# Performance work log

Measured on AMD Instinct MI355X. Metric: run time of the kernel, lower is better.

## Reference

```python
import jax, jax.numpy as jnp
import numpy as np

# Paged/ragged causal prefill attention (FlashInfer wrapper.run semantics),
# modeled as equal-length batched causal GQA attention.
B, S = 2, 2048          # batch, seq_len (T = B*S tokens, flattened)
H, HKV, D = 32, 8, 128  # query heads, kv heads, head dim
G = H // HKV            # GQA group size
SCALE = 0.08838834764831845  # 1/sqrt(D)


def setup_inputs() -> dict:
    key = jax.random.key(0)
    kq, kk, kv = jax.random.split(key, 3)
    q = jax.random.normal(kq, (B * S, H * D), dtype=jnp.float32)
    k = jax.random.normal(kk, (B * S, HKV * D), dtype=jnp.float32)
    v = jax.random.normal(kv, (B * S, HKV * D), dtype=jnp.float32)
    return {"q": q, "k": k, "v": v}


def reference(q, k, v):
    # q: [T, H*D] -> [B, S, HKV, G, D]; k, v: [T, HKV*D] -> [B, S, HKV, D]
    qh = q.reshape(B, S, HKV, G, D)
    kh = k.reshape(B, S, HKV, D)
    vh = v.reshape(B, S, HKV, D)
    # GQA attention scores: [B, HKV, G, Sq, Sk]
    scores = jnp.einsum('bqhgd,bkhd->bhgqk', qh, kh) * SCALE
    causal = jnp.tril(jnp.ones((S, S), dtype=bool))  # query attends to keys <= its position
    scores = jnp.where(causal, scores, jnp.finfo(scores.dtype).min)
    probs = jax.nn.softmax(scores, axis=-1)
    out = jnp.einsum('bhgqk,bkhd->bqhgd', probs, vh)
    # back to flattened token layout [T, H*D]
    return out.reshape(B * S, H * D)
```

## Files before the change

kernel.cpp:

```cpp
#include <hip/hip_runtime.h>


#define B_   2
#define S_   2048
#define H_   32
#define HKV_ 8
#define D_   128
#define SCALEF 0.08838834764831845f
#define COEF  (SCALEF * 1.44269504088896340736f)
#define DEFER_THR 8.0f

typedef float          f32x4 __attribute__((ext_vector_type(4)));
typedef __bf16         bf16x4 __attribute__((ext_vector_type(4)));
typedef __bf16         bf16x8 __attribute__((ext_vector_type(8)));
typedef unsigned short u16x8 __attribute__((ext_vector_type(8)));

#define MFMA16(a, b, c) __builtin_amdgcn_mfma_f32_16x16x32_bf16((a), (b), (c), 0, 0, 0)

#if defined(__has_builtin)
#if __has_builtin(__builtin_amdgcn_exp2f)
#define EXP2F(x) __builtin_amdgcn_exp2f(x)
#endif
#endif
#ifndef EXP2F
#define EXP2F(x) exp2f(x)
#endif

static __device__ __forceinline__ unsigned short f2bf(float f) {
  unsigned int u = __builtin_bit_cast(unsigned int, f);
  u = (u + 0x7fffu + ((u >> 16) & 1u)) >> 16;
  return (unsigned short)u;
}

static __device__ __forceinline__ void load_lds16(const void* g, void* l) {
  __builtin_amdgcn_global_load_lds(
      (const __attribute__((address_space(1))) void*)g,
      (__attribute__((address_space(3))) void*)l, 16, 0, 0);
}

static __device__ __forceinline__ float swz_x16(float v) {
  return __builtin_bit_cast(
      float, __builtin_amdgcn_ds_swizzle(__builtin_bit_cast(int, v), 0x401F));
}
static __device__ __forceinline__ float bperm_f(int byteaddr, float v) {
  return __builtin_bit_cast(
      float,
      __builtin_amdgcn_ds_bpermute(byteaddr, __builtin_bit_cast(int, v)));
}

__global__ __launch_bounds__(256) void k_convert_kernel(
    const float* __restrict__ k, unsigned short* __restrict__ kbf) {
  int t = blockIdx.x * 256 + threadIdx.x;
  int o = t * 8;
  int d = o & (D_ - 1);
  int s = (o >> 7) & (S_ - 1);
  int bh = o >> 18;
  int b = bh >> 3, hkv = bh & 7;
  const float* src = k + (size_t)(b * S_ + s) * (HKV_ * D_) + hkv * D_ + d;
  f32x4 x0 = *(const f32x4*)src;
  f32x4 x1 = *(const f32x4*)(src + 4);
  u16x8 w;
  w[0] = f2bf(x0[0]); w[1] = f2bf(x0[1]); w[2] = f2bf(x0[2]); w[3] = f2bf(x0[3]);
  w[4] = f2bf(x1[0]); w[5] = f2bf(x1[1]); w[6] = f2bf(x1[2]); w[7] = f2bf(x1[3]);
  *(u16x8*)(kbf + o) = w;
}

__global__ __launch_bounds__(256) void vt_transpose_kernel(
    const float* __restrict__ v, unsigned short* __restrict__ vt) {
  __shared__ float tile[32][65];
  const int tid = threadIdx.x;
  const int s0 = blockIdx.x * 64;
  const int d0 = blockIdx.y * 32;
  const int bh = blockIdx.z;
  const float* src = v + (size_t)(bh >> 3) * S_ * (HKV_ * D_) + (bh & 7) * D_;
#pragma unroll
  for (int it = 0; it < 8; ++it) {
    int idx = it * 256 + tid;
    int sl = idx >> 5, dl = idx & 31;
    tile[dl][sl] = src[(size_t)(s0 + sl) * (HKV_ * D_) + d0 + dl];
  }
  __syncthreads();
  unsigned int* dst = (unsigned int*)vt;
#pragma unroll
  for (int it = 0; it < 4; ++it) {
    int idx = it * 256 + tid;
    int dl = idx >> 5, sp = idx & 31;
    unsigned int w = (unsigned int)f2bf(tile[dl][2 * sp]) |
                     ((unsigned int)f2bf(tile[dl][2 * sp + 1]) << 16);
    dst[(((size_t)bh * D_ + d0 + dl) * S_ + s0 + 2 * sp) >> 1] = w;
  }
}

#define PSTR 36

__global__ __launch_bounds__(256, 4) void attn_kernel(
    const float* __restrict__ qg, const unsigned short* __restrict__ kbfg,
    const unsigned short* __restrict__ vtg, float* __restrict__ outg) {
  __shared__ unsigned short KL[2][32 * 128];
  __shared__ unsigned short VL[2][128 * 32];
  __shared__ unsigned short PL[4][16 * PSTR];

  const int tid = threadIdx.x;
  const int wave = tid >> 6, lane = tid & 63;
  const int l15 = lane & 15, quad = lane >> 4;
  const int a32 = ((lane ^ 32) << 2);
  const int rowa = quad << 4;

  const int xb = (int)blockIdx.x;
  const int b = (int)(blockIdx.y >> 5), h = (int)(blockIdx.y & 31);
  const int hkv = h >> 2;

  const unsigned short* kbf = kbfg + (size_t)(b * HKV_ + hkv) * S_ * D_;
  const unsigned short* vtb = vtg + (size_t)(b * HKV_ + hkv) * D_ * S_;

  const f32x4 zero4 = {0.f, 0.f, 0.f, 0.f};
  const float NEG_INF = -__builtin_huge_valf();

  auto stage = [&](int kt, int buf) {
#pragma unroll
    for (int j = 0; j < 2; ++j) {
      int si = wave * 128 + j * 64 + lane;
      int kr = si >> 4, pc = si & 15;
      int lc = pc ^ (kr & 15);
      load_lds16(kbf + (size_t)(kt * 32 + kr) * D_ + lc * 8,
                 &KL[buf][(wave * 128 + j * 64) * 8]);
    }
#pragma unroll
    for (int j = 0; j < 2; ++j) {
      int si = wave * 128 + j * 64 + lane;
      int dr = si >> 2, pc = si & 3;
      int lc = pc ^ ((dr >> 1) & 3);
      load_lds16(vtb + (size_t)dr * S_ + kt * 32 + lc * 8,
                 &VL[buf][(wave * 128 + j * 64) * 8]);
    }
  };

  for (int ph = 0; ph < 2; ++ph) {
    const int qb = ph ? (31 - xb) : xb;
    const int qbase = qb * 64 + wave * 16;
    const int qgp = qbase + l15;

    bf16x8 qf[4];
#pragma unroll
    for (int ch = 0; ch < 4; ++ch) {
      const float* p = qg + (size_t)(b * S_ + qbase + l15) * (H_ * D_) +
                       h * D_ + ch * 32 + quad * 8;
      f32x4 x0 = *(const f32x4*)p;
      f32x4 x1 = *(const f32x4*)(p + 4);
      bf16x8 t;
      t[0] = (__bf16)(x0[0] * COEF); t[1] = (__bf16)(x0[1] * COEF);
      t[2] = (__bf16)(x0[2] * COEF); t[3] = (__bf16)(x0[3] * COEF);
      t[4] = (__bf16)(x1[0] * COEF); t[5] = (__bf16)(x1[1] * COEF);
      t[6] = (__bf16)(x1[2] * COEF); t[7] = (__bf16)(x1[3] * COEF);
      qf[ch] = t;
    }

    f32x4 acc[8];
#pragma unroll
    for (int dt = 0; dt < 8; ++dt) acc[dt] = zero4;
    float mrow = NEG_INF;
    float lsum = 0.f;

    const int nkt = qb * 2 + 2;

    stage(0, 0);
    __syncthreads();

#define KITER(KT, CUR)                                                        \
  do {                                                                        \
    const int kt_ = (KT);                                                     \
    if (kt_ + 1 < nkt) stage(kt_ + 1, (CUR) ^ 1);                             \
    if (kt_ * 32 <= qbase + 15) {                                             \
      f32x4 sc[2] = {zero4, zero4};                                           \
      __builtin_amdgcn_s_setprio(1);                                          \
      _Pragma("unroll") for (int h2 = 0; h2 < 2; ++h2) {                      \
        const int row = h2 * 16 + l15;                                        \
        _Pragma("unroll") for (int ch = 0; ch < 4; ++ch) {                    \
          const int pc = (ch * 4 + quad) ^ l15;               \
          u16x8 kf = *(const u16x8*)&KL[(CUR)][row * D_ + pc * 8];            \
          sc[h2] = MFMA16(__builtin_bit_cast(bf16x8, kf), qf[ch], sc[h2]);    \
        }                                                                     \
      }                                                                       \
      __builtin_amdgcn_s_setprio(0);                                          \
      const int kb0 = kt_ * 32;                                               \
          \
      _Pragma("unroll") for (int h2 = 0; h2 < 2; ++h2) {                      \
        if (kb0 + h2 * 16 + 15 > qbase) {                                     \
          int kb2 = kb0 + h2 * 16 + quad * 4;                                 \
          _Pragma("unroll") for (int r = 0; r < 4; ++r) {                     \
            if (kb2 + r > qgp) sc[h2][r] = NEG_INF;                           \
          }                                                                   \
        }                                                                     \
      }                                                                       \
         \
      float l8 = fmaxf(fmaxf(fmaxf(sc[0][0], sc[0][1]),                       \
                             fmaxf(sc[0][2], sc[0][3])),                      \
                       fmaxf(fmaxf(sc[1][0], sc[1][1]),                       \
                             fmaxf(sc[1][2], sc[1][3])));                     \
      if (!__all(l8 <= mrow + DEFER_THR)) {                                   \
        float t = fmaxf(l8, swz_x16(l8));             \
        t = fmaxf(t, bperm_f(a32, t));                                        \
        float mn = fmaxf(mrow, t);                                            \
        float al = EXP2F(mrow - mn);                                          \
        mrow = mn;                                                            \
        lsum *= al;                                                           \
        f32x4 av;       \
        _Pragma("unroll") for (int r = 0; r < 4; ++r)                         \
            av[r] = bperm_f(rowa + (r << 2), al);                             \
        _Pragma("unroll") for (int dt = 0; dt < 8; ++dt)                      \
            _Pragma("unroll") for (int r = 0; r < 4; ++r)                     \
                acc[dt][r] *= av[r];                                          \
      }                                                                       \
                         \
      _Pragma("unroll") for (int h2 = 0; h2 < 2; ++h2)                        \
          _Pragma("unroll") for (int r = 0; r < 4; ++r)                       \
              sc[h2][r] = EXP2F(sc[h2][r] - mrow);                            \
      lsum += ((sc[0][0] + sc[0][1]) + (sc[0][2] + sc[0][3])) +               \
              ((sc[1][0] + sc[1][1]) + (sc[1][2] + sc[1][3]));                \
            \
      {                                                                       \
        bf16x4 w0, w1;                                                        \
        w0[0] = (__bf16)sc[0][0]; w0[1] = (__bf16)sc[0][1];                   \
        w0[2] = (__bf16)sc[0][2]; w0[3] = (__bf16)sc[0][3];                   \
        w1[0] = (__bf16)sc[1][0]; w1[1] = (__bf16)sc[1][1];                   \
        w1[2] = (__bf16)sc[1][2]; w1[3] = (__bf16)sc[1][3];                   \
        *(bf16x4*)&PL[wave][l15 * PSTR + quad * 4] = w0;                      \
        *(bf16x4*)&PL[wave][l15 * PSTR + 16 + quad * 4] = w1;                 \
      }                                                                       \
             \
      {                                                                       \
        bf16x4 p0 = *(const bf16x4*)&PL[wave][l15 * PSTR + quad * 8];         \
        bf16x4 p1 = *(const bf16x4*)&PL[wave][l15 * PSTR + quad * 8 + 4];     \
        bf16x8 pb = __builtin_shufflevector(p0, p1, 0, 1, 2, 3, 4, 5, 6, 7);  \
        const int vsw = (quad ^ ((l15 >> 1) & 3)) * 8;                        \
        __builtin_amdgcn_s_setprio(1);                                        \
        _Pragma("unroll") for (int dt = 0; dt < 8; ++dt) {                    \
          u16x8 vf = *(const u16x8*)&VL[(CUR)][(dt * 16 + l15) * 32 + vsw];   \
          acc[dt] = MFMA16(pb, __builtin_bit_cast(bf16x8, vf), acc[dt]);      \
        }                                                                     \
        __builtin_amdgcn_s_setprio(0);                                        \
      }                                                                       \
    }                                                                         \
    __syncthreads();  \
  } while (0)

    for (int kt = 0; kt < nkt; kt += 2) {
      KITER(kt, 0);
      KITER(kt + 1, 1);
    }
#undef KITER

    float s = lsum;
    s += swz_x16(s);
    s += bperm_f(a32, s);
    float linv = 1.0f / s;
    f32x4 inv;
#pragma unroll
    for (int r = 0; r < 4; ++r) inv[r] = bperm_f(rowa + (r << 2), linv);
#pragma unroll
    for (int dt = 0; dt < 8; ++dt)
#pragma unroll
      for (int r = 0; r < 4; ++r)
        outg[(size_t)(b * S_ + qbase + quad * 4 + r) * (H_ * D_) +
             h * D_ + dt * 16 + l15] = acc[dt][r] * inv[r];
  }
}

extern "C" void kernel_launch(void* const* d_in, const int* in_sizes, int n_in,
                              void* d_out, int out_size, void* d_ws,
                              size_t ws_size, hipStream_t stream) {
  const float* q = (const float*)d_in[0];
  const float* k = (const float*)d_in[1];
  const float* v = (const float*)d_in[2];
  float* out = (float*)d_out;
  unsigned short* kws = (unsigned short*)d_ws;
  unsigned short* vtws = kws + (size_t)B_ * HKV_ * S_ * D_;

  k_convert_kernel<<<(B_ * S_ * HKV_ * D_ / 8) / 256, 256, 0, stream>>>(k, kws);

  dim3 g1(S_ / 64, D_ / 32, B_ * HKV_);
  vt_transpose_kernel<<<g1, 256, 0, stream>>>(v, vtws);

  dim3 g2(16, B_ * H_);
  attn_kernel<<<g2, 256, 0, stream>>>(q, kws, vtws, out);
}
```

Before: 233.2 us.

## Permute K rows to keep P in registers, fuse prep kernels, remap blocks to XCDs

New measurement: 244.5 us. +4.9%, slower.

```diff
diff --git a/kernel.cpp b/kernel.cpp
--- a/kernel.cpp
+++ b/kernel.cpp
@@ -48,57 +48,56 @@
       __builtin_amdgcn_ds_bpermute(byteaddr, __builtin_bit_cast(int, v)));
 }
 
-__global__ __launch_bounds__(256) void k_convert_kernel(
-    const float* __restrict__ k, unsigned short* __restrict__ kbf) {
-  int t = blockIdx.x * 256 + threadIdx.x;
-  int o = t * 8;
-  int d = o & (D_ - 1);
-  int s = (o >> 7) & (S_ - 1);
-  int bh = o >> 18;
-  int b = bh >> 3, hkv = bh & 7;
-  const float* src = k + (size_t)(b * S_ + s) * (HKV_ * D_) + hkv * D_ + d;
-  f32x4 x0 = *(const f32x4*)src;
-  f32x4 x1 = *(const f32x4*)(src + 4);
-  u16x8 w;
-  w[0] = f2bf(x0[0]); w[1] = f2bf(x0[1]); w[2] = f2bf(x0[2]); w[3] = f2bf(x0[3]);
-  w[4] = f2bf(x1[0]); w[5] = f2bf(x1[1]); w[6] = f2bf(x1[2]); w[7] = f2bf(x1[3]);
-  *(u16x8*)(kbf + o) = w;
-}
-
-__global__ __launch_bounds__(256) void vt_transpose_kernel(
-    const float* __restrict__ v, unsigned short* __restrict__ vt) {
+__global__ __launch_bounds__(256) void prep_kernel(
+    const float* __restrict__ k, const float* __restrict__ v,
+    unsigned short* __restrict__ kbf, unsigned short* __restrict__ vt) {
   __shared__ float tile[32][65];
   const int tid = threadIdx.x;
-  const int s0 = blockIdx.x * 64;
-  const int d0 = blockIdx.y * 32;
-  const int bh = blockIdx.z;
-  const float* src = v + (size_t)(bh >> 3) * S_ * (HKV_ * D_) + (bh & 7) * D_;
-#pragma unroll
-  for (int it = 0; it < 8; ++it) {
-    int idx = it * 256 + tid;
-    int sl = idx >> 5, dl = idx & 31;
-    tile[dl][sl] = src[(size_t)(s0 + sl) * (HKV_ * D_) + d0 + dl];
+  const int gid = (int)blockIdx.x;
+  if (gid < 2048) {
+    int t = gid * 256 + tid;
+    int o = t * 8;
+    int d = o & (D_ - 1);
+    int s = (o >> 7) & (S_ - 1);
+    int bh = o >> 18;
+    int b = bh >> 3, hkv = bh & 7;
+    const float* src = k + (size_t)(b * S_ + s) * (HKV_ * D_) + hkv * D_ + d;
+    f32x4 x0 = *(const f32x4*)src;
+    f32x4 x1 = *(const f32x4*)(src + 4);
+    u16x8 w;
+    w[0] = f2bf(x0[0]); w[1] = f2bf(x0[1]); w[2] = f2bf(x0[2]); w[3] = f2bf(x0[3]);
+    w[4] = f2bf(x1[0]); w[5] = f2bf(x1[1]); w[6] = f2bf(x1[2]); w[7] = f2bf(x1[3]);
+    *(u16x8*)(kbf + o) = w;
+  } else {
+    const int t = gid - 2048;
+    const int s0 = (t & 31) * 64;
+    const int d0 = ((t >> 5) & 3) * 32;
+    const int bh = t >> 7;
+    const float* src = v + (size_t)(bh >> 3) * S_ * (HKV_ * D_) + (bh & 7) * D_;
+#pragma unroll
+    for (int it = 0; it < 8; ++it) {
+      int idx = it * 256 + tid;
+      int sl = idx >> 5, dl = idx & 31;
+      tile[dl][sl] = src[(size_t)(s0 + sl) * (HKV_ * D_) + d0 + dl];
+    }
+    __syncthreads();
+    unsigned int* dst = (unsigned int*)vt;
+#pragma unroll
+    for (int it = 0; it < 4; ++it) {
+      int idx = it * 256 + tid;
+      int dl = idx >> 5, sp = idx & 31;
+      unsigned int w = (unsigned int)f2bf(tile[dl][2 * sp]) |
+                       ((unsigned int)f2bf(tile[dl][2 * sp + 1]) << 16);
+      dst[(((size_t)bh * D_ + d0 + dl) * S_ + s0 + 2 * sp) >> 1] = w;
+    }
   }
-  __syncthreads();
-  unsigned int* dst = (unsigned int*)vt;
-#pragma unroll
-  for (int it = 0; it < 4; ++it) {
-    int idx = it * 256 + tid;
-    int dl = idx >> 5, sp = idx & 31;
-    unsigned int w = (unsigned int)f2bf(tile[dl][2 * sp]) |
-                     ((unsigned int)f2bf(tile[dl][2 * sp + 1]) << 16);
-    dst[(((size_t)bh * D_ + d0 + dl) * S_ + s0 + 2 * sp) >> 1] = w;
-  }
-}
-
-#define PSTR 36
-
-__global__ __launch_bounds__(256, 4) void attn_kernel(
+}
+
+__global__ __launch_bounds__(256, 5) void attn_kernel(
     const float* __restrict__ qg, const unsigned short* __restrict__ kbfg,
     const unsigned short* __restrict__ vtg, float* __restrict__ outg) {
   __shared__ unsigned short KL[2][32 * 128];
   __shared__ unsigned short VL[2][128 * 32];
-  __shared__ unsigned short PL[4][16 * PSTR];
 
   const int tid = threadIdx.x;
   const int wave = tid >> 6, lane = tid & 63;
@@ -106,9 +105,14 @@
   const int a32 = ((lane ^ 32) << 2);
   const int rowa = quad << 4;
 
-  const int xb = (int)blockIdx.x;
-  const int b = (int)(blockIdx.y >> 5), h = (int)(blockIdx.y & 31);
-  const int hkv = h >> 2;
+  const int id = (int)blockIdx.x + 16 * (int)blockIdx.y;
+  const int xcd = id & 7, slot = id >> 3;
+  const int bhkv = xcd * 2 + (slot >> 6);
+  const int inner = slot & 63;
+  const int g = inner >> 4;
+  const int xb = inner & 15;
+  const int b = bhkv >> 3, hkv = bhkv & 7;
+  const int h = hkv * 4 + g;
 
   const unsigned short* kbf = kbfg + (size_t)(b * HKV_ + hkv) * S_ * D_;
   const unsigned short* vtb = vtg + (size_t)(b * HKV_ + hkv) * D_ * S_;
@@ -122,7 +126,8 @@
       int si = wave * 128 + j * 64 + lane;
       int kr = si >> 4, pc = si & 15;
       int lc = pc ^ (kr & 15);
-      load_lds16(kbf + (size_t)(kt * 32 + kr) * D_ + lc * 8,
+      int gs = ((kr & 15) >> 2) * 8 + ((kr >> 4) << 2) + (kr & 3);
+      load_lds16(kbf + (size_t)(kt * 32 + gs) * D_ + lc * 8,
                  &KL[buf][(wave * 128 + j * 64) * 8]);
     }
 #pragma unroll
@@ -183,16 +188,16 @@
       }                                                                       \
       __builtin_amdgcn_s_setprio(0);                                          \
       const int kb0 = kt_ * 32;                                               \
-          \
+                       \
       _Pragma("unroll") for (int h2 = 0; h2 < 2; ++h2) {                      \
-        if (kb0 + h2 * 16 + 15 > qbase) {                                     \
-          int kb2 = kb0 + h2 * 16 + quad * 4;                                 \
+        if (kb0 + 27 + h2 * 4 > qbase) {                                      \
+          int kb2 = kb0 + quad * 8 + h2 * 4;                                  \
           _Pragma("unroll") for (int r = 0; r < 4; ++r) {                     \
             if (kb2 + r > qgp) sc[h2][r] = NEG_INF;                           \
           }                                                                   \
         }                                                                     \
       }                                                                       \
-         \
+                      \
       float l8 = fmaxf(fmaxf(fmaxf(sc[0][0], sc[0][1]),                       \
                              fmaxf(sc[0][2], sc[0][3])),                      \
                        fmaxf(fmaxf(sc[1][0], sc[1][1]),                       \
@@ -217,21 +222,14 @@
               sc[h2][r] = EXP2F(sc[h2][r] - mrow);                            \
       lsum += ((sc[0][0] + sc[0][1]) + (sc[0][2] + sc[0][3])) +               \
               ((sc[1][0] + sc[1][1]) + (sc[1][2] + sc[1][3]));                \
-            \
+             \
+      bf16x8 pb;                                                              \
+      pb[0] = (__bf16)sc[0][0]; pb[1] = (__bf16)sc[0][1];                     \
+      pb[2] = (__bf16)sc[0][2]; pb[3] = (__bf16)sc[0][3];                     \
+      pb[4] = (__bf16)sc[1][0]; pb[5] = (__bf16)sc[1][1];                     \
+      pb[6] = (__bf16)sc[1][2]; pb[7] = (__bf16)sc[1][3];                     \
+                       \
       {                                                                       \
-        bf16x4 w0, w1;                                                        \
-        w0[0] = (__bf16)sc[0][0]; w0[1] = (__bf16)sc[0][1];                   \
-        w0[2] = (__bf16)sc[0][2]; w0[3] = (__bf16)sc[0][3];                   \
-        w1[0] = (__bf16)sc[1][0]; w1[1] = (__bf16)sc[1][1];                   \
-        w1[2] = (__bf16)sc[1][2]; w1[3] = (__bf16)sc[1][3];                   \
-        *(bf16x4*)&PL[wave][l15 * PSTR + quad * 4] = w0;                      \
-        *(bf16x4*)&PL[wave][l15 * PSTR + 16 + quad * 4] = w1;                 \
-      }                                                                       \
-             \
-      {                                                                       \
-        bf16x4 p0 = *(const bf16x4*)&PL[wave][l15 * PSTR + quad * 8];         \
-        bf16x4 p1 = *(const bf16x4*)&PL[wave][l15 * PSTR + quad * 8 + 4];     \
-        bf16x8 pb = __builtin_shufflevector(p0, p1, 0, 1, 2, 3, 4, 5, 6, 7);  \
         const int vsw = (quad ^ ((l15 >> 1) & 3)) * 8;                        \
         __builtin_amdgcn_s_setprio(1);                                        \
         _Pragma("unroll") for (int dt = 0; dt < 8; ++dt) {                    \
@@ -276,10 +274,7 @@
   unsigned short* kws = (unsigned short*)d_ws;
   unsigned short* vtws = kws + (size_t)B_ * HKV_ * S_ * D_;
 
-  k_convert_kernel<<<(B_ * S_ * HKV_ * D_ / 8) / 256, 256, 0, stream>>>(k, kws);
-
-  dim3 g1(S_ / 64, D_ / 32, B_ * HKV_);
-  vt_transpose_kernel<<<g1, 256, 0, stream>>>(v, vtws);
+  prep_kernel<<<4096, 256, 0, stream>>>(k, v, kws, vtws);
 
   dim3 g2(16, B_ * H_);
   attn_kernel<<<g2, 256, 0, stream>>>(q, kws, vtws, out);
```
